# Kernel optimization log

Hardware: AMD Instinct MI355X
Metric: run time of the kernel (lower is better)

## Reference

```python
import jax, jax.numpy as jnp
import numpy as np

VOCAB = 100000
EMB = 256
NUM_SAMPLED = 256
BATCH = 16384


def _log_uniform_prob(ids, range_max):
    # tf log_uniform_candidate_sampler: P(k) = (log(k+2) - log(k+1)) / log(range_max + 1)
    ids = ids.astype(jnp.float32)
    return (jnp.log(ids + 2.0) - jnp.log(ids + 1.0)) / jnp.log(float(range_max) + 1.0)


def setup_inputs() -> dict:
    key = jax.random.key(0)
    k1, k2, k3, k4, k5 = jax.random.split(key, 5)
    embeddings = jax.random.uniform(k1, (VOCAB, EMB), jnp.float32, -1.0, 1.0)
    # truncated_normal(stddev=0.03) init for the NCE decoder weights
    nce_weights = jax.random.truncated_normal(k2, -2.0, 2.0, (VOCAB, EMB), jnp.float32) * 0.03
    nce_biases = jnp.zeros((VOCAB,), jnp.float32)
    inputs = jax.random.randint(k3, (BATCH,), 0, VOCAB, jnp.int64)
    train_labels = jax.random.randint(k4, (BATCH, 1), 0, VOCAB, jnp.int64)
    sampled_ids = jax.random.randint(k5, (NUM_SAMPLED,), 0, VOCAB, jnp.int64)
    return {
        "embeddings": embeddings,
        "nce_weights": nce_weights,
        "nce_biases": nce_biases,
        "inputs": inputs,
        "train_labels": train_labels,
        "sampled_ids": sampled_ids,
    }


def _sigmoid_xent(logits, label):
    # stable sigmoid cross-entropy with logits
    return jnp.maximum(logits, 0.0) - logits * label + jnp.log1p(jnp.exp(-jnp.abs(logits)))


def reference(embeddings, nce_weights, nce_biases, inputs, train_labels, sampled_ids):
    # embedding lookup: [B, E]
    embed = embeddings[inputs]

    labels = train_labels[:, 0]  # num_true = 1
    true_w = nce_weights[labels]          # [B, E]
    true_b = nce_biases[labels]           # [B]
    true_logits = jnp.sum(embed * true_w, axis=-1) + true_b
    true_logits = true_logits - jnp.log(NUM_SAMPLED * _log_uniform_prob(labels, VOCAB))

    samp_w = nce_weights[sampled_ids]     # [S, E]
    samp_b = nce_biases[sampled_ids]      # [S]
    sampled_logits = jnp.einsum("be,se->bs", embed, samp_w) + samp_b
    sampled_logits = sampled_logits - jnp.log(NUM_SAMPLED * _log_uniform_prob(sampled_ids, VOCAB))

    per_example = _sigmoid_xent(true_logits, 1.0) + jnp.sum(_sigmoid_xent(sampled_logits, 0.0), axis=-1)
    nce_cost = jnp.mean(per_example)
    return embed, nce_cost
```

## Files before the change

kernel.cpp:

```cpp
#include <hip/hip_runtime.h>
#include <math.h>

#define EMB 256
#define NS 256
#define BATCH_SZ 16384
#define ROWS 16
#define LDA 264

typedef __attribute__((ext_vector_type(8))) __bf16 bf16x8;
typedef __attribute__((ext_vector_type(4))) float  f32x4;

__device__ __forceinline__ float log_corr(int id) {
    const float INV_LOG_RANGE = 1.0f / 11.5129354649f;
    float p = log1pf(1.0f / ((float)id + 1.0f)) * INV_LOG_RANGE;
    return logf((float)NS * p);
}
__device__ __forceinline__ unsigned short f2bf(float x) {
    unsigned int u = __float_as_uint(x);
    u += 0x7FFFu + ((u >> 16) & 1u);
    return (unsigned short)(u >> 16);
}
__device__ __forceinline__ float bf2f(unsigned short b) {
    return __uint_as_float(((unsigned int)b) << 16);
}

extern "C" __global__ void __launch_bounds__(64)
nce_prep(const float* __restrict__ nce_weights,
         const float* __restrict__ nce_biases,
         const int*   __restrict__ sampled_ids,
         unsigned short* __restrict__ Bsw,
         float* __restrict__ scws,
         float* __restrict__ out_cost)
{
    const int tid = blockIdx.x * 64 + threadIdx.x;
    const int s   = tid >> 5;
    const int u   = tid & 31;
    const int sid = sampled_ids[s];
    const float4* wr = (const float4*)(nce_weights + (size_t)sid * EMB + u * 8);
    float4 a = wr[0], b = wr[1];
    unsigned short o[8] = { f2bf(a.x), f2bf(a.y), f2bf(a.z), f2bf(a.w),
                            f2bf(b.x), f2bf(b.y), f2bf(b.z), f2bf(b.w) };
    const int T = s >> 4, kb = u >> 2;
    const int lane = ((u & 3) << 4) | (s & 15);
    unsigned short* dst = Bsw + ((size_t)((T * 8 + kb) * 64 + lane)) * 8;
    *(ushort4*)(dst)     = *(ushort4*)&o[0];
    *(ushort4*)(dst + 4) = *(ushort4*)&o[4];
    if (u == 0) scws[s] = nce_biases[sid] - log_corr(sid);
    if (tid == 0) *out_cost = 0.0f;
}

extern "C" __global__ void __launch_bounds__(256)
nce_main(const float* __restrict__ embeddings,
         const float* __restrict__ nce_weights,
         const float* __restrict__ nce_biases,
         const int*   __restrict__ inputs,
         const int*   __restrict__ labels,
         const unsigned short* __restrict__ Bsw,
         const float* __restrict__ scws,
         float* __restrict__ out_embed,
         float* __restrict__ out_cost)
{
    __shared__ unsigned short A[ROWS * LDA];
    __shared__ float sc_l[NS];
    __shared__ float wpart[4];

    const int t    = threadIdx.x;
    const int lane = t & 63;
    const int wv   = t >> 6;
    const int b0   = blockIdx.x * ROWS;

    sc_l[t] = scws[t];

    #pragma unroll
    for (int i = 0; i < 4; ++i) {
        int r = i * 4 + wv;
        int b = b0 + r;
        int idx = inputs[b];
        const float4 v = *(const float4*)(embeddings + (size_t)idx * EMB + lane * 4);
        *(float4*)(out_embed + (size_t)b * EMB + lane * 4) = v;
        ushort4 o;
        o.x = f2bf(v.x); o.y = f2bf(v.y); o.z = f2bf(v.z); o.w = f2bf(v.w);
        *(ushort4*)(A + r * LDA + lane * 4) = o;
    }
    __syncthreads();

    float myloss = 0.0f;

    #pragma unroll
    for (int j = 0; j < 4; ++j) {
        int r = wv * 4 + j;
        int b = b0 + r;
        int lab = labels[b];
        float4 w4 = *(const float4*)(nce_weights + (size_t)lab * EMB + lane * 4);
        ushort4 e = *(const ushort4*)(A + r * LDA + lane * 4);
        float p = bf2f(e.x) * w4.x + bf2f(e.y) * w4.y +
                  bf2f(e.z) * w4.z + bf2f(e.w) * w4.w;
        #pragma unroll
        for (int o = 32; o > 0; o >>= 1) p += __shfl_down(p, o, 64);
        if (lane == 0) {
            float tl = p + nce_biases[lab] - log_corr(lab);
            myloss += fmaxf(tl, 0.0f) - tl + log1pf(expf(-fabsf(tl)));
        }
    }

    const int l15 = lane & 15;
    const int lq  = lane >> 4;
    const unsigned short* Arow = A + l15 * LDA + lq * 8;
    const bf16x8* Bv = (const bf16x8*)Bsw;

    f32x4 acc[4];
    #pragma unroll
    for (int tt = 0; tt < 4; ++tt) acc[tt] = (f32x4){0.f, 0.f, 0.f, 0.f};

    #pragma unroll
    for (int kb = 0; kb < 8; ++kb) {
        bf16x8 af = *(const bf16x8*)(Arow + kb * 32);
        #pragma unroll
        for (int tt = 0; tt < 4; ++tt) {
            int T = wv * 4 + tt;
            bf16x8 bfm = Bv[(T * 8 + kb) * 64 + lane];
            acc[tt] = __builtin_amdgcn_mfma_f32_16x16x32_bf16(af, bfm, acc[tt], 0, 0, 0);
        }
    }

    #pragma unroll
    for (int tt = 0; tt < 4; ++tt) {
        float scv = sc_l[wv * 64 + tt * 16 + l15];
        #pragma unroll
        for (int i = 0; i < 4; ++i) {
            float x = acc[tt][i] + scv;
            myloss += fmaxf(x, 0.0f) + log1pf(expf(-fabsf(x)));
        }
    }

    #pragma unroll
    for (int o = 32; o > 0; o >>= 1) myloss += __shfl_down(myloss, o, 64);
    if (lane == 0) wpart[wv] = myloss;
    __syncthreads();
    if (t == 0) {
        float s = wpart[0] + wpart[1] + wpart[2] + wpart[3];
        atomicAdd(out_cost, s * (1.0f / (float)BATCH_SZ));
    }
}

extern "C" void kernel_launch(void* const* d_in, const int* in_sizes, int n_in,
                              void* d_out, int out_size, void* d_ws, size_t ws_size,
                              hipStream_t stream) {
    const float* embeddings  = (const float*)d_in[0];
    const float* nce_weights = (const float*)d_in[1];
    const float* nce_biases  = (const float*)d_in[2];
    const int*   inputs      = (const int*)d_in[3];
    const int*   labels      = (const int*)d_in[4];
    const int*   sampled_ids = (const int*)d_in[5];

    float* out      = (float*)d_out;
    float* out_cost = out + (size_t)BATCH_SZ * EMB;

    unsigned short* Bsw  = (unsigned short*)d_ws;
    float*          scws = (float*)((char*)d_ws + NS * EMB * sizeof(unsigned short));

    nce_prep<<<NS * 32 / 64, 64, 0, stream>>>(
        nce_weights, nce_biases, sampled_ids, Bsw, scws, out_cost);

    nce_main<<<BATCH_SZ / ROWS, 256, 0, stream>>>(
        embeddings, nce_weights, nce_biases, inputs, labels,
        Bsw, scws, out, out_cost);
}
```

Before: 217.6 us.

## Split sampled columns across two blocks and compute true logits via MFMA

Each group of 16 rows is now handled by two blocks, each computing half of the sampled-logit columns, which doubles the grid and halves the per-wave MFMA work. Embedding rows are gathered redundantly by both blocks, but only one writes the embed output. The true-label dot products are folded into an extra MFMA on wave 0 of split 0, with the label weights converted to bf16. Input indices are loaded once per wave and broadcast with shuffles, and launch bounds request 8 blocks per CU. The cost is twice the embedding gather traffic and twice as many atomic adds.

New measurement: 217.5 us. No clear change (-0.0%).

```diff
diff --git a/kernel.cpp b/kernel.cpp
--- a/kernel.cpp
+++ b/kernel.cpp
@@ -19,9 +19,6 @@
     unsigned int u = __float_as_uint(x);
     u += 0x7FFFu + ((u >> 16) & 1u);
     return (unsigned short)(u >> 16);
-}
-__device__ __forceinline__ float bf2f(unsigned short b) {
-    return __uint_as_float(((unsigned int)b) << 16);
 }
 
 extern "C" __global__ void __launch_bounds__(64)
@@ -49,7 +46,7 @@
     if (tid == 0) *out_cost = 0.0f;
 }
 
-extern "C" __global__ void __launch_bounds__(256)
+extern "C" __global__ void __launch_bounds__(256, 8)
 nce_main(const float* __restrict__ embeddings,
          const float* __restrict__ nce_weights,
          const float* __restrict__ nce_biases,
@@ -64,73 +61,79 @@
     __shared__ float sc_l[NS];
     __shared__ float wpart[4];
 
-    const int t    = threadIdx.x;
-    const int lane = t & 63;
-    const int wv   = t >> 6;
-    const int b0   = blockIdx.x * ROWS;
+    const int t     = threadIdx.x;
+    const int lane  = t & 63;
+    const int wv    = t >> 6;
+    const int split = blockIdx.x & 1;
+    const int b0    = (blockIdx.x >> 1) * ROWS;
+    const int l15   = lane & 15;
+    const int lq    = lane >> 4;
+    const bool w0s0 = (wv == 0) && (split == 0);
 
     sc_l[t] = scws[t];
+
+    const int idxv = inputs[b0 + l15];
+    int labv = 0;
+    if (w0s0) labv = labels[b0 + l15];
 
     #pragma unroll
     for (int i = 0; i < 4; ++i) {
         int r = i * 4 + wv;
-        int b = b0 + r;
-        int idx = inputs[b];
+        int idx = __shfl(idxv, r, 64);
         const float4 v = *(const float4*)(embeddings + (size_t)idx * EMB + lane * 4);
-        *(float4*)(out_embed + (size_t)b * EMB + lane * 4) = v;
+        if (split == 0)
+            *(float4*)(out_embed + (size_t)(b0 + r) * EMB + lane * 4) = v;
         ushort4 o;
         o.x = f2bf(v.x); o.y = f2bf(v.y); o.z = f2bf(v.z); o.w = f2bf(v.w);
         *(ushort4*)(A + r * LDA + lane * 4) = o;
     }
     __syncthreads();
 
-    float myloss = 0.0f;
-
-    #pragma unroll
-    for (int j = 0; j < 4; ++j) {
-        int r = wv * 4 + j;
-        int b = b0 + r;
-        int lab = labels[b];
-        float4 w4 = *(const float4*)(nce_weights + (size_t)lab * EMB + lane * 4);
-        ushort4 e = *(const ushort4*)(A + r * LDA + lane * 4);
-        float p = bf2f(e.x) * w4.x + bf2f(e.y) * w4.y +
-                  bf2f(e.z) * w4.z + bf2f(e.w) * w4.w;
-        #pragma unroll
-        for (int o = 32; o > 0; o >>= 1) p += __shfl_down(p, o, 64);
-        if (lane == 0) {
-            float tl = p + nce_biases[lab] - log_corr(lab);
-            myloss += fmaxf(tl, 0.0f) - tl + log1pf(expf(-fabsf(tl)));
-        }
-    }
-
-    const int l15 = lane & 15;
-    const int lq  = lane >> 4;
     const unsigned short* Arow = A + l15 * LDA + lq * 8;
     const bf16x8* Bv = (const bf16x8*)Bsw;
+    const int T0 = split * 8 + wv * 2;
 
-    f32x4 acc[4];
-    #pragma unroll
-    for (int tt = 0; tt < 4; ++tt) acc[tt] = (f32x4){0.f, 0.f, 0.f, 0.f};
+    f32x4 acc0 = (f32x4){0.f, 0.f, 0.f, 0.f};
+    f32x4 acc1 = (f32x4){0.f, 0.f, 0.f, 0.f};
+    f32x4 tacc = (f32x4){0.f, 0.f, 0.f, 0.f};
+
+    const float* wtrue = nce_weights + (size_t)labv * EMB + lq * 8;
 
     #pragma unroll
     for (int kb = 0; kb < 8; ++kb) {
         bf16x8 af = *(const bf16x8*)(Arow + kb * 32);
-        #pragma unroll
-        for (int tt = 0; tt < 4; ++tt) {
-            int T = wv * 4 + tt;
-            bf16x8 bfm = Bv[(T * 8 + kb) * 64 + lane];
-            acc[tt] = __builtin_amdgcn_mfma_f32_16x16x32_bf16(af, bfm, acc[tt], 0, 0, 0);
+        bf16x8 bf0 = Bv[((T0 + 0) * 8 + kb) * 64 + lane];
+        bf16x8 bf1 = Bv[((T0 + 1) * 8 + kb) * 64 + lane];
+        acc0 = __builtin_amdgcn_mfma_f32_16x16x32_bf16(af, bf0, acc0, 0, 0, 0);
+        acc1 = __builtin_amdgcn_mfma_f32_16x16x32_bf16(af, bf1, acc1, 0, 0, 0);
+        if (w0s0) {
+            const float4* wr = (const float4*)(wtrue + kb * 32);
+            float4 a = wr[0], b = wr[1];
+            unsigned short o[8] __attribute__((aligned(16))) =
+                { f2bf(a.x), f2bf(a.y), f2bf(a.z), f2bf(a.w),
+                  f2bf(b.x), f2bf(b.y), f2bf(b.z), f2bf(b.w) };
+            bf16x8 tb = *(bf16x8*)o;
+            tacc = __builtin_amdgcn_mfma_f32_16x16x32_bf16(af, tb, tacc, 0, 0, 0);
         }
     }
 
-    #pragma unroll
-    for (int tt = 0; tt < 4; ++tt) {
-        float scv = sc_l[wv * 64 + tt * 16 + l15];
+    float myloss = 0.0f;
+
+    {
+        float sc0 = sc_l[(T0 + 0) * 16 + l15];
+        float sc1 = sc_l[(T0 + 1) * 16 + l15];
         #pragma unroll
         for (int i = 0; i < 4; ++i) {
-            float x = acc[tt][i] + scv;
-            myloss += fmaxf(x, 0.0f) + log1pf(expf(-fabsf(x)));
+            float x0 = acc0[i] + sc0;
+            float x1 = acc1[i] + sc1;
+            myloss += fmaxf(x0, 0.0f) + log1pf(expf(-fabsf(x0)));
+            myloss += fmaxf(x1, 0.0f) + log1pf(expf(-fabsf(x1)));
         }
+    }
+
+    if (w0s0 && (lq == (l15 >> 2))) {
+        float tl = tacc[l15 & 3] + nce_biases[labv] - log_corr(labv);
+        myloss += fmaxf(tl, 0.0f) - tl + log1pf(expf(-fabsf(tl)));
     }
 
     #pragma unroll
@@ -162,7 +165,7 @@
     nce_prep<<<NS * 32 / 64, 64, 0, stream>>>(
         nce_weights, nce_biases, sampled_ids, Bsw, scws, out_cost);
 
-    nce_main<<<BATCH_SZ / ROWS, 256, 0, stream>>>(
+    nce_main<<<(BATCH_SZ / ROWS) * 2, 256, 0, stream>>>(
         embeddings, nce_weights, nce_biases, inputs, labels,
         Bsw, scws, out, out_cost);
 }
```

## Replace atomic cost accumulation with per-block partials and a final reduction kernel

Applied to the files above, without the earlier changes.

Each main block now writes its loss partial to a workspace array, and a new single-block kernel sums the partials, replacing the per-block float atomicAdd. Input and label indices are loaded once per wave and broadcast with shuffles instead of separate scalar loads. Softplus now uses the fast __expf/__logf intrinsics, and launch bounds request 4 blocks per CU. The extra kernel adds launch overhead, and the fast math slightly changes precision for large |x|.

New measurement: 204.7 us. 5.9% less time.

```diff
diff --git a/kernel.cpp b/kernel.cpp
--- a/kernel.cpp
+++ b/kernel.cpp
@@ -6,6 +6,7 @@
 #define BATCH_SZ 16384
 #define ROWS 16
 #define LDA 264
+#define NBLK (BATCH_SZ / ROWS)
 
 typedef __attribute__((ext_vector_type(8))) __bf16 bf16x8;
 typedef __attribute__((ext_vector_type(4))) float  f32x4;
@@ -23,14 +24,16 @@
 __device__ __forceinline__ float bf2f(unsigned short b) {
     return __uint_as_float(((unsigned int)b) << 16);
 }
+__device__ __forceinline__ float softplus_neg(float a) {
+    return __logf(1.0f + __expf(-a));
+}
 
 extern "C" __global__ void __launch_bounds__(64)
 nce_prep(const float* __restrict__ nce_weights,
          const float* __restrict__ nce_biases,
          const int*   __restrict__ sampled_ids,
          unsigned short* __restrict__ Bsw,
-         float* __restrict__ scws,
-         float* __restrict__ out_cost)
+         float* __restrict__ scws)
 {
     const int tid = blockIdx.x * 64 + threadIdx.x;
     const int s   = tid >> 5;
@@ -46,10 +49,9 @@
     *(ushort4*)(dst)     = *(ushort4*)&o[0];
     *(ushort4*)(dst + 4) = *(ushort4*)&o[4];
     if (u == 0) scws[s] = nce_biases[sid] - log_corr(sid);
-    if (tid == 0) *out_cost = 0.0f;
 }
 
-extern "C" __global__ void __launch_bounds__(256)
+extern "C" __global__ void __launch_bounds__(256, 4)
 nce_main(const float* __restrict__ embeddings,
          const float* __restrict__ nce_weights,
          const float* __restrict__ nce_biases,
@@ -58,7 +60,7 @@
          const unsigned short* __restrict__ Bsw,
          const float* __restrict__ scws,
          float* __restrict__ out_embed,
-         float* __restrict__ out_cost)
+         float* __restrict__ partials)
 {
     __shared__ unsigned short A[ROWS * LDA];
     __shared__ float sc_l[NS];
@@ -68,16 +70,20 @@
     const int lane = t & 63;
     const int wv   = t >> 6;
     const int b0   = blockIdx.x * ROWS;
+    const int l15  = lane & 15;
+    const int lq   = lane >> 4;
 
     sc_l[t] = scws[t];
+
+    const int idxv = inputs[b0 + l15];
+    const int labv = labels[b0 + l15];
 
     #pragma unroll
     for (int i = 0; i < 4; ++i) {
         int r = i * 4 + wv;
-        int b = b0 + r;
-        int idx = inputs[b];
+        int idx = __shfl(idxv, r, 64);
         const float4 v = *(const float4*)(embeddings + (size_t)idx * EMB + lane * 4);
-        *(float4*)(out_embed + (size_t)b * EMB + lane * 4) = v;
+        *(float4*)(out_embed + (size_t)(b0 + r) * EMB + lane * 4) = v;
         ushort4 o;
         o.x = f2bf(v.x); o.y = f2bf(v.y); o.z = f2bf(v.z); o.w = f2bf(v.w);
         *(ushort4*)(A + r * LDA + lane * 4) = o;
@@ -89,8 +95,7 @@
     #pragma unroll
     for (int j = 0; j < 4; ++j) {
         int r = wv * 4 + j;
-        int b = b0 + r;
-        int lab = labels[b];
+        int lab = __shfl(labv, r, 64);
         float4 w4 = *(const float4*)(nce_weights + (size_t)lab * EMB + lane * 4);
         ushort4 e = *(const ushort4*)(A + r * LDA + lane * 4);
         float p = bf2f(e.x) * w4.x + bf2f(e.y) * w4.y +
@@ -99,12 +104,10 @@
         for (int o = 32; o > 0; o >>= 1) p += __shfl_down(p, o, 64);
         if (lane == 0) {
             float tl = p + nce_biases[lab] - log_corr(lab);
-            myloss += fmaxf(tl, 0.0f) - tl + log1pf(expf(-fabsf(tl)));
+            myloss += fmaxf(tl, 0.0f) - tl + softplus_neg(fabsf(tl));
         }
     }
 
-    const int l15 = lane & 15;
-    const int lq  = lane >> 4;
     const unsigned short* Arow = A + l15 * LDA + lq * 8;
     const bf16x8* Bv = (const bf16x8*)Bsw;
 
@@ -129,7 +132,7 @@
         #pragma unroll
         for (int i = 0; i < 4; ++i) {
             float x = acc[tt][i] + scv;
-            myloss += fmaxf(x, 0.0f) + log1pf(expf(-fabsf(x)));
+            myloss += fmaxf(x, 0.0f) + softplus_neg(fabsf(x));
         }
     }
 
@@ -137,10 +140,26 @@
     for (int o = 32; o > 0; o >>= 1) myloss += __shfl_down(myloss, o, 64);
     if (lane == 0) wpart[wv] = myloss;
     __syncthreads();
-    if (t == 0) {
-        float s = wpart[0] + wpart[1] + wpart[2] + wpart[3];
-        atomicAdd(out_cost, s * (1.0f / (float)BATCH_SZ));
-    }
+    if (t == 0)
+        partials[blockIdx.x] = wpart[0] + wpart[1] + wpart[2] + wpart[3];
+}
+
+extern "C" __global__ void __launch_bounds__(256)
+nce_final(const float* __restrict__ partials, float* __restrict__ out_cost)
+{
+    __shared__ float wpart[4];
+    const int t    = threadIdx.x;
+    const int lane = t & 63;
+    const int wv   = t >> 6;
+    float s = 0.0f;
+    #pragma unroll
+    for (int i = 0; i < NBLK / 256; ++i) s += partials[i * 256 + t];
+    #pragma unroll
+    for (int o = 32; o > 0; o >>= 1) s += __shfl_down(s, o, 64);
+    if (lane == 0) wpart[wv] = s;
+    __syncthreads();
+    if (t == 0)
+        *out_cost = (wpart[0] + wpart[1] + wpart[2] + wpart[3]) * (1.0f / (float)BATCH_SZ);
 }
 
 extern "C" void kernel_launch(void* const* d_in, const int* in_sizes, int n_in,
@@ -156,13 +175,16 @@
     float* out      = (float*)d_out;
     float* out_cost = out + (size_t)BATCH_SZ * EMB;
 
-    unsigned short* Bsw  = (unsigned short*)d_ws;
-    float*          scws = (float*)((char*)d_ws + NS * EMB * sizeof(unsigned short));
+    unsigned short* Bsw      = (unsigned short*)d_ws;
+    float*          scws     = (float*)((char*)d_ws + NS * EMB * sizeof(unsigned short));
+    float*          partials = scws + NS;
 
     nce_prep<<<NS * 32 / 64, 64, 0, stream>>>(
-        nce_weights, nce_biases, sampled_ids, Bsw, scws, out_cost);
+        nce_weights, nce_biases, sampled_ids, Bsw, scws);
 
-    nce_main<<<BATCH_SZ / ROWS, 256, 0, stream>>>(
+    nce_main<<<NBLK, 256, 0, stream>>>(
         embeddings, nce_weights, nce_biases, inputs, labels,
-        Bsw, scws, out, out_cost);
+        Bsw, scws, out, partials);
+
+    nce_final<<<1, 256, 0, stream>>>(partials, out_cost);
 }
```
